# Kernel optimization log

Hardware: AMD Instinct MI355X
Metric: run time of the kernel (lower is better)

The kernel has to match this reference:

```python
import jax, jax.numpy as jnp
import numpy as np

K = 3  # kernel height/width (filter_size = (1, 3, 3), nF = 9)


def _extract_patches(x):
    """x: [B, C, H, W] -> patches [B, C, H, W, K*K], matching the identity
    grouped conv2d (cross-correlation) with padding=1 in the original:
    patch index i = dy*K + dx corresponds to x[c, h+dy-1, w+dx-1]."""
    B, C, H, W = x.shape
    xp = jnp.pad(x, ((0, 0), (0, 0), (1, 1), (1, 1)))
    # fixed K*K=9 offsets: small static loop, not a data-dim loop
    return jnp.stack(
        [xp[:, :, dy:dy + H, dx:dx + W] for dy in range(K) for dx in range(K)],
        axis=-1,
    )


def setup_inputs() -> dict:
    key = jax.random.key(0)
    k1, k2 = jax.random.split(key)
    B, C, H, W = 4, 128, 180, 320
    nF = K * K
    x = jax.random.normal(k1, (B, C, H, W), dtype=jnp.float32)
    filters = jax.random.normal(k2, (B, nF, H, W), dtype=jnp.float32)
    return {"x": x, "filters": filters}


def reference(x, filters):
    """x: [B, 128, H, W]; filters: [B, 9, H, W]. Returns [B, 128, H, W].
    Equivalent to: im2col (identity grouped conv) then per-pixel matmul
    [128, 9] @ [9, 1] at every spatial location."""
    patches = _extract_patches(x)                       # [B, C, H, W, 9]
    f = jnp.transpose(filters, (0, 2, 3, 1))            # [B, H, W, 9]
    out = jnp.einsum('bchwf,bhwf->bchw', patches, f)    # per-pixel dot
    return out
```

## Files before the change

### kernel.cpp

```cpp
#include <hip/hip_runtime.h>


#define CC 128
#define HH 180
#define WW 320
#define W4 80
#define NF 9

__global__ __launch_bounds__(256) void duf_kernel(
    const float* __restrict__ x,
    const float* __restrict__ f,
    float* __restrict__ out,
    int total)
{
    int n = blockIdx.x * 256 + threadIdx.x;
    if (n >= total) return;

    int w4 = n % W4;
    int t  = n / W4;
    int c  = t % CC;
    t /= CC;
    int h  = t % HH;
    int b  = t / HH;

    const float4* x4 = (const float4*)x;
    const float4* f4 = (const float4*)f;

    float4 fr[NF];
    int fbase = (b * NF * HH + h) * W4 + w4;
#pragma unroll
    for (int i = 0; i < NF; ++i)
        fr[i] = f4[fbase + i * (HH * W4)];

    float4 acc = make_float4(0.f, 0.f, 0.f, 0.f);
    int xchan4 = (b * CC + c) * HH * W4;

#pragma unroll
    for (int dy = 0; dy < 3; ++dy) {
        int hh = h + dy - 1;
        float4 xc = make_float4(0.f, 0.f, 0.f, 0.f);
        float xl = 0.f, xr = 0.f;
        if (hh >= 0 && hh < HH) {
            int rb4 = xchan4 + hh * W4;
            xc = x4[rb4 + w4];
            const float* rowf = x + (size_t)rb4 * 4;
            if (w4 > 0)      xl = rowf[w4 * 4 - 1];
            if (w4 < W4 - 1) xr = rowf[w4 * 4 + 4];
        }
        float4 f0 = fr[3 * dy + 0];
        float4 f1 = fr[3 * dy + 1];
        float4 f2 = fr[3 * dy + 2];
        acc.x = fmaf(f0.x, xl,   fmaf(f1.x, xc.x, fmaf(f2.x, xc.y, acc.x)));
        acc.y = fmaf(f0.y, xc.x, fmaf(f1.y, xc.y, fmaf(f2.y, xc.z, acc.y)));
        acc.z = fmaf(f0.z, xc.y, fmaf(f1.z, xc.z, fmaf(f2.z, xc.w, acc.z)));
        acc.w = fmaf(f0.w, xc.z, fmaf(f1.w, xc.w, fmaf(f2.w, xr,   acc.w)));
    }

    ((float4*)out)[(size_t)((b * CC + c) * HH + h) * W4 + w4] = acc;
}

extern "C" void kernel_launch(void* const* d_in, const int* in_sizes, int n_in,
                              void* d_out, int out_size, void* d_ws, size_t ws_size,
                              hipStream_t stream) {
    const float* x = (const float*)d_in[0];
    const float* f = (const float*)d_in[1];
    float* out = (float*)d_out;

    int B = in_sizes[0] / (CC * HH * WW);
    int total = B * CC * HH * W4;
    int blocks = (total + 255) / 256;

    duf_kernel<<<blocks, 256, 0, stream>>>(x, f, out, total);
}
```

Baseline: 284.8 us.

## Tile per (batch,row) block with shared-memory staging of filters and x rows

Each block now handles one (b,h) row across all 128 channels, loading the 9 filter rows once into shared memory and registers instead of once per channel. Channels are processed in chunks of 8: the three neighbouring x rows are staged into padded shared memory, and each thread computes two channels. This removes the redundant filter reloads and the scalar halo loads. The cost is barriers per chunk and only 720 blocks, which limits parallelism and gives no overlap between the loads and the compute.

```diff
diff --git a/kernel.cpp b/kernel.cpp
--- a/kernel.cpp
+++ b/kernel.cpp
@@ -6,57 +6,87 @@
 #define WW 320
 #define W4 80
 #define NF 9
+#define CHUNK 8
+#define NCHUNK (CC / CHUNK)
+#define RS 328
+#define XS_CH (3 * RS)
+#define NT 320
 
-__global__ __launch_bounds__(256) void duf_kernel(
+__global__ __launch_bounds__(NT, 4) void duf_kernel(
     const float* __restrict__ x,
     const float* __restrict__ f,
-    float* __restrict__ out,
-    int total)
+    float* __restrict__ out)
 {
-    int n = blockIdx.x * 256 + threadIdx.x;
-    if (n >= total) return;
+    __shared__ float fs[NF * WW];
+    __shared__ float xs[CHUNK * 3 * RS];
 
-    int w4 = n % W4;
-    int t  = n / W4;
-    int c  = t % CC;
-    t /= CC;
-    int h  = t % HH;
-    int b  = t / HH;
+    const int t = threadIdx.x;
+    const int h = blockIdx.x % HH;
+    const int b = blockIdx.x / HH;
 
-    const float4* x4 = (const float4*)x;
-    const float4* f4 = (const float4*)f;
+    for (int idx = t; idx < NF * W4; idx += NT) {
+        int i  = idx / W4;
+        int w4 = idx % W4;
+        ((float4*)fs)[idx] =
+            ((const float4*)f)[((size_t)(b * NF + i) * HH + h) * W4 + w4];
+    }
+    for (int idx = t; idx < CHUNK * 3 * 2; idx += NT) {
+        int r = idx >> 1;
+        int side = idx & 1;
+        ((float4*)&xs[r * RS + side * (RS - 4)])[0] =
+            make_float4(0.f, 0.f, 0.f, 0.f);
+    }
+
+    const int w4    = t % W4;
+    const int cslot = t / W4;
 
     float4 fr[NF];
-    int fbase = (b * NF * HH + h) * W4 + w4;
+
+    for (int chunk = 0; chunk < NCHUNK; ++chunk) {
+        if (chunk) __syncthreads();
+
+        const int c0 = chunk * CHUNK;
 #pragma unroll
-    for (int i = 0; i < NF; ++i)
-        fr[i] = f4[fbase + i * (HH * W4)];
+        for (int it = 0; it < 6; ++it) {
+            int idx = it * NT + t;
+            int lw4 = idx % W4;
+            int rr  = (idx / W4) % 3;
+            int ch  = idx / 240;
+            int hh  = h - 1 + rr;
+            float4 v = make_float4(0.f, 0.f, 0.f, 0.f);
+            if (hh >= 0 && hh < HH)
+                v = ((const float4*)x)[((size_t)(b * CC + c0 + ch) * HH + hh) * W4 + lw4];
+            ((float4*)&xs[ch * XS_CH + rr * RS + 4])[lw4] = v;
+        }
+        __syncthreads();
 
-    float4 acc = make_float4(0.f, 0.f, 0.f, 0.f);
-    int xchan4 = (b * CC + c) * HH * W4;
+        if (chunk == 0) {
+#pragma unroll
+            for (int i = 0; i < NF; ++i)
+                fr[i] = ((const float4*)&fs[i * WW])[w4];
+        }
 
 #pragma unroll
-    for (int dy = 0; dy < 3; ++dy) {
-        int hh = h + dy - 1;
-        float4 xc = make_float4(0.f, 0.f, 0.f, 0.f);
-        float xl = 0.f, xr = 0.f;
-        if (hh >= 0 && hh < HH) {
-            int rb4 = xchan4 + hh * W4;
-            xc = x4[rb4 + w4];
-            const float* rowf = x + (size_t)rb4 * 4;
-            if (w4 > 0)      xl = rowf[w4 * 4 - 1];
-            if (w4 < W4 - 1) xr = rowf[w4 * 4 + 4];
+        for (int j = 0; j < 2; ++j) {
+            int ch = cslot * 2 + j;
+            float4 acc = make_float4(0.f, 0.f, 0.f, 0.f);
+#pragma unroll
+            for (int dy = 0; dy < 3; ++dy) {
+                const float4* rp = (const float4*)&xs[ch * XS_CH + dy * RS];
+                float4 A = rp[w4];
+                float4 B = rp[w4 + 1];
+                float4 C = rp[w4 + 2];
+                float4 f0 = fr[3 * dy + 0];
+                float4 f1 = fr[3 * dy + 1];
+                float4 f2 = fr[3 * dy + 2];
+                acc.x = fmaf(f0.x, A.w, fmaf(f1.x, B.x, fmaf(f2.x, B.y, acc.x)));
+                acc.y = fmaf(f0.y, B.x, fmaf(f1.y, B.y, fmaf(f2.y, B.z, acc.y)));
+                acc.z = fmaf(f0.z, B.y, fmaf(f1.z, B.z, fmaf(f2.z, B.w, acc.z)));
+                acc.w = fmaf(f0.w, B.z, fmaf(f1.w, B.w, fmaf(f2.w, C.x, acc.w)));
+            }
+            ((float4*)out)[((size_t)(b * CC + c0 + ch) * HH + h) * W4 + w4] = acc;
         }
-        float4 f0 = fr[3 * dy + 0];
-        float4 f1 = fr[3 * dy + 1];
-        float4 f2 = fr[3 * dy + 2];
-        acc.x = fmaf(f0.x, xl,   fmaf(f1.x, xc.x, fmaf(f2.x, xc.y, acc.x)));
-        acc.y = fmaf(f0.y, xc.x, fmaf(f1.y, xc.y, fmaf(f2.y, xc.z, acc.y)));
-        acc.z = fmaf(f0.z, xc.y, fmaf(f1.z, xc.z, fmaf(f2.z, xc.w, acc.z)));
-        acc.w = fmaf(f0.w, xc.z, fmaf(f1.w, xc.w, fmaf(f2.w, xr,   acc.w)));
     }
-
-    ((float4*)out)[(size_t)((b * CC + c) * HH + h) * W4 + w4] = acc;
 }
 
 extern "C" void kernel_launch(void* const* d_in, const int* in_sizes, int n_in,
@@ -67,8 +97,7 @@
     float* out = (float*)d_out;
 
     int B = in_sizes[0] / (CC * HH * WW);
-    int total = B * CC * HH * W4;
-    int blocks = (total + 255) / 256;
+    int blocks = B * HH;
 
-    duf_kernel<<<blocks, 256, 0, stream>>>(x, f, out, total);
+    duf_kernel<<<blocks, NT, 0, stream>>>(x, f, out);
 }
```

Result: slower. 307.4 us (+8.0%).

## Compute two output rows and eight channels per thread to reuse filter and input rows

Applied to the files above, without the earlier changes.

Each thread now produces two vertically adjacent output rows for eight channels. It loads the filter values for both rows once and reuses them across the channels. Each thread reads four input rows instead of six, and the edge neighbours come from float4 loads with masking instead of scalar loads. The aim is to cut redundant filter and input traffic, at the cost of fewer threads, more registers and no bounds guard on the total (the grid size must divide exactly).

```diff
diff --git a/kernel.cpp b/kernel.cpp
--- a/kernel.cpp
+++ b/kernel.cpp
@@ -3,60 +3,76 @@
 
 #define CC 128
 #define HH 180
-#define WW 320
 #define W4 80
 #define NF 9
+#define CPT 8
+#define H2 (HH / 2)
+#define NCG (CC / CPT)
+
+__device__ __forceinline__ void fma_row(float4& acc, float4 f0, float4 f1,
+                                        float4 f2, float4 A, float4 B, float4 C) {
+    acc.x = fmaf(f0.x, A.w, fmaf(f1.x, B.x, fmaf(f2.x, B.y, acc.x)));
+    acc.y = fmaf(f0.y, B.x, fmaf(f1.y, B.y, fmaf(f2.y, B.z, acc.y)));
+    acc.z = fmaf(f0.z, B.y, fmaf(f1.z, B.z, fmaf(f2.z, B.w, acc.z)));
+    acc.w = fmaf(f0.w, B.z, fmaf(f1.w, B.w, fmaf(f2.w, C.x, acc.w)));
+}
 
 __global__ __launch_bounds__(256) void duf_kernel(
     const float* __restrict__ x,
     const float* __restrict__ f,
-    float* __restrict__ out,
-    int total)
+    float* __restrict__ out)
 {
     int n = blockIdx.x * 256 + threadIdx.x;
-    if (n >= total) return;
-
     int w4 = n % W4;
     int t  = n / W4;
-    int c  = t % CC;
-    t /= CC;
-    int h  = t % HH;
-    int b  = t / HH;
+    int cg = t % NCG;
+    t /= NCG;
+    int h2 = t % H2;
+    int b  = t / H2;
+    int h  = h2 * 2;
 
     const float4* x4 = (const float4*)x;
     const float4* f4 = (const float4*)f;
+    float4* o4 = (float4*)out;
 
-    float4 fr[NF];
-    int fbase = (b * NF * HH + h) * W4 + w4;
+    float4 fr0[NF], fr1[NF];
+    size_t fbase = ((size_t)(b * NF) * HH + h) * W4 + w4;
 #pragma unroll
-    for (int i = 0; i < NF; ++i)
-        fr[i] = f4[fbase + i * (HH * W4)];
-
-    float4 acc = make_float4(0.f, 0.f, 0.f, 0.f);
-    int xchan4 = (b * CC + c) * HH * W4;
-
-#pragma unroll
-    for (int dy = 0; dy < 3; ++dy) {
-        int hh = h + dy - 1;
-        float4 xc = make_float4(0.f, 0.f, 0.f, 0.f);
-        float xl = 0.f, xr = 0.f;
-        if (hh >= 0 && hh < HH) {
-            int rb4 = xchan4 + hh * W4;
-            xc = x4[rb4 + w4];
-            const float* rowf = x + (size_t)rb4 * 4;
-            if (w4 > 0)      xl = rowf[w4 * 4 - 1];
-            if (w4 < W4 - 1) xr = rowf[w4 * 4 + 4];
-        }
-        float4 f0 = fr[3 * dy + 0];
-        float4 f1 = fr[3 * dy + 1];
-        float4 f2 = fr[3 * dy + 2];
-        acc.x = fmaf(f0.x, xl,   fmaf(f1.x, xc.x, fmaf(f2.x, xc.y, acc.x)));
-        acc.y = fmaf(f0.y, xc.x, fmaf(f1.y, xc.y, fmaf(f2.y, xc.z, acc.y)));
-        acc.z = fmaf(f0.z, xc.y, fmaf(f1.z, xc.z, fmaf(f2.z, xc.w, acc.z)));
-        acc.w = fmaf(f0.w, xc.z, fmaf(f1.w, xc.w, fmaf(f2.w, xr,   acc.w)));
+    for (int i = 0; i < NF; ++i) {
+        fr0[i] = f4[fbase + (size_t)i * HH * W4];
+        fr1[i] = f4[fbase + (size_t)i * HH * W4 + W4];
     }
 
-    ((float4*)out)[(size_t)((b * CC + c) * HH + h) * W4 + w4] = acc;
+    const int wl = (w4 > 0) ? w4 - 1 : 0;
+    const int wr = (w4 < W4 - 1) ? w4 + 1 : w4;
+    const bool at_l = (w4 == 0);
+    const bool at_r = (w4 == W4 - 1);
+
+    const int c0 = cg * CPT;
+    for (int cc = 0; cc < CPT; ++cc) {
+        const size_t xb = (size_t)(b * CC + c0 + cc) * HH * W4;
+        float4 a0 = make_float4(0.f, 0.f, 0.f, 0.f);
+        float4 a1 = make_float4(0.f, 0.f, 0.f, 0.f);
+#pragma unroll
+        for (int r = 0; r < 4; ++r) {
+            int hr = h - 1 + r;
+            float4 A = make_float4(0.f, 0.f, 0.f, 0.f);
+            float4 B = A, C = A;
+            if (hr >= 0 && hr < HH) {
+                size_t rb = xb + (size_t)hr * W4;
+                A = x4[rb + wl];
+                B = x4[rb + w4];
+                C = x4[rb + wr];
+                if (at_l) A.w = 0.f;
+                if (at_r) C.x = 0.f;
+            }
+            if (r < 3) fma_row(a0, fr0[3*r  ], fr0[3*r+1], fr0[3*r+2], A, B, C);
+            if (r > 0) fma_row(a1, fr1[3*r-3], fr1[3*r-2], fr1[3*r-1], A, B, C);
+        }
+        size_t ob = ((size_t)(b * CC + c0 + cc) * HH + h) * W4 + w4;
+        o4[ob]      = a0;
+        o4[ob + W4] = a1;
+    }
 }
 
 extern "C" void kernel_launch(void* const* d_in, const int* in_sizes, int n_in,
@@ -66,9 +82,7 @@
     const float* f = (const float*)d_in[1];
     float* out = (float*)d_out;
 
-    int B = in_sizes[0] / (CC * HH * WW);
-    int total = B * CC * HH * W4;
-    int blocks = (total + 255) / 256;
-
-    duf_kernel<<<blocks, 256, 0, stream>>>(x, f, out, total);
+    int B = in_sizes[0] / (CC * HH * W4 * 4);
+    int total = B * H2 * NCG * W4;
+    duf_kernel<<<total / 256, 256, 0, stream>>>(x, f, out);
 }
```

Measured after the change: 240.5 us. -15.6%, faster.
